# Optimization experiments

Measured on AMD Instinct MI355X. Metric: run time of the kernel, lower is better.

The kernel has to match this reference:

```python
import jax, jax.numpy as jnp
import numpy as np

K = 20          # neighbors
BN_EPS = 1e-5


def _knn_idx(x, k):
    """x: [B, C, N] -> idx of k nearest neighbors [B, N, k] (by squared distance, self included)."""
    xx = jnp.sum(x * x, axis=1)                       # [B, N]
    inner = jnp.einsum('bcn,bcm->bnm', x, x)          # [B, N, N]
    neg_sqdist = 2.0 * inner - xx[:, :, None] - xx[:, None, :]
    return jax.lax.top_k(neg_sqdist, k)[1]            # [B, N, k]


def _graph_feature(x, k):
    """x: [B, C, N] -> edge features cat(x_j - x_i, x_i): [B, 2C, N, k]."""
    idx = _knn_idx(x, k)                              # [B, N, k]
    xT = x.transpose(0, 2, 1)                         # [B, N, C]
    nbrs = jax.vmap(lambda xt, ii: xt[ii])(xT, idx)   # [B, N, k, C] gather
    center = xT[:, :, None, :]                        # [B, N, 1, C]
    feat = jnp.concatenate(
        [nbrs - center, jnp.broadcast_to(center, nbrs.shape)], axis=-1)  # [B, N, k, 2C]
    return feat.transpose(0, 3, 1, 2)                 # [B, 2C, N, k]


def _conv_bn_lrelu(feat, W, gamma, beta, mean, var):
    """1x1 Conv2d (no bias) + BatchNorm (given stats) + LeakyReLU(0.2). feat: [B, Cin, N, k]."""
    y = jnp.einsum('oc,bcnk->bonk', W, feat)
    scale = (gamma / jnp.sqrt(var + BN_EPS))[None, :, None, None]
    y = (y - mean[None, :, None, None]) * scale + beta[None, :, None, None]
    return jnp.where(y > 0, y, 0.2 * y)


def setup_inputs() -> dict:
    key = jax.random.key(0)
    ks = list(jax.random.split(key, 32))
    B, N = 8, 1024
    f32 = jnp.float32

    def w(kk, o, i):
        return jax.random.normal(kk, (o, i), dtype=f32) / np.sqrt(i)

    def bn(k1, k2, k3, k4, c):
        g = jax.random.uniform(k1, (c,), dtype=f32, minval=0.5, maxval=1.5)
        b = jax.random.normal(k2, (c,), dtype=f32) * 0.05
        m = jax.random.normal(k3, (c,), dtype=f32) * 0.05
        v = jax.random.uniform(k4, (c,), dtype=f32, minval=0.5, maxval=1.5)
        return g, b, m, v

    x = jax.random.normal(ks[0], (B, N, 3), dtype=f32)
    W0 = w(ks[1], 64, 6);    g0, b0, m0, v0 = bn(ks[2], ks[3], ks[4], ks[5], 64)
    W1 = w(ks[6], 128, 128); g1, b1, m1, v1 = bn(ks[7], ks[8], ks[9], ks[10], 128)
    W2 = w(ks[11], 256, 256); g2, b2, m2, v2 = bn(ks[12], ks[13], ks[14], ks[15], 256)
    Wf = w(ks[16], 512, 896); gf, bf, mf, vf = bn(ks[17], ks[18], ks[19], ks[20], 512)
    We = w(ks[21], 256, 512)
    return dict(x=x,
                W0=W0, g0=g0, b0=b0, m0=m0, v0=v0,
                W1=W1, g1=g1, b1=b1, m1=m1, v1=v1,
                W2=W2, g2=g2, b2=b2, m2=m2, v2=v2,
                Wf=Wf, gf=gf, bf=bf, mf=mf, vf=vf,
                We=We)


def reference(x, W0, g0, b0, m0, v0, W1, g1, b1, m1, v1,
              W2, g2, b2, m2, v2, Wf, gf, bf, mf, vf, We):
    h = x.transpose(0, 2, 1)                          # [B, 3, N]
    outs = []
    for (W, g, b, m, v) in ((W0, g0, b0, m0, v0),
                            (W1, g1, b1, m1, v1),
                            (W2, g2, b2, m2, v2)):
        gfeat = _graph_feature(h, K)                  # [B, 2C, N, k]
        y = _conv_bn_lrelu(gfeat, W, g, b, m, v)      # [B, Cout, N, k]
        h = y.mean(axis=-1)                           # max-free EdgeConv pool over k
        outs.append(h)
    cat = jnp.concatenate(outs, axis=1)               # [B, 448, N]
    gfeat = _graph_feature(cat, K)                    # [B, 896, N, k]
    y = _conv_bn_lrelu(gfeat, Wf, gf, bf, mf, vf)     # [B, 512, N, k]
    pooled = y.mean(axis=-1).mean(axis=-1)            # [B, 512] (pool over k then N)
    return pooled @ We.T                              # [B, num_features]
```

## Files before the change

### kernel.cpp

```cpp
#include <hip/hip_runtime.h>
#include <cstdint>

#define KNN 20
#define BV 8
#define NV 1024

template <int CTRL>
__device__ __forceinline__ unsigned dppmax(unsigned x) {
    unsigned m = (unsigned)__builtin_amdgcn_update_dpp((int)x, (int)x, CTRL, 0xf, 0xf, false);
    return (x > m) ? x : m;
}
template <int CTRL>
__device__ __forceinline__ unsigned dppmin(unsigned x) {
    unsigned m = (unsigned)__builtin_amdgcn_update_dpp((int)x, (int)x, CTRL, 0xf, 0xf, false);
    return (x < m) ? x : m;
}
__device__ __forceinline__ unsigned wave_max_u32(unsigned x) {
    x = dppmax<0xB1>(x); x = dppmax<0x4E>(x); x = dppmax<0x141>(x);
    x = dppmax<0x140>(x); x = dppmax<0x142>(x); x = dppmax<0x143>(x);
    return (unsigned)__builtin_amdgcn_readlane((int)x, 63);
}
__device__ __forceinline__ unsigned wave_min_u32(unsigned x) {
    x = dppmin<0xB1>(x); x = dppmin<0x4E>(x); x = dppmin<0x141>(x);
    x = dppmin<0x140>(x); x = dppmin<0x142>(x); x = dppmin<0x143>(x);
    return (unsigned)__builtin_amdgcn_readlane((int)x, 63);
}

__global__ __launch_bounds__(256) void k_transpose(const float* __restrict__ x, float* __restrict__ hx) {
    int id = blockIdx.x * 256 + threadIdx.x;
    if (id >= BV * 3 * NV) return;
    int n = id % NV;
    int c = (id / NV) % 3;
    int b = id / (3 * NV);
    hx[id] = x[(b * NV + n) * 3 + c];
}

__global__ __launch_bounds__(256) void k_xx(const float* __restrict__ h, float* __restrict__ xx,
                                            int C, int bstride) {
    int id = blockIdx.x * 256 + threadIdx.x;
    int n = id % NV, b = id / NV;
    if (b >= BV) return;
    const float* hp = h + (size_t)b * bstride + n;
    float s = 0.f;
    for (int c = 0; c < C; ++c) { float v = hp[(size_t)c * NV]; s += v * v; }
    xx[b * NV + n] = s;
}

__global__ __launch_bounds__(512, 4) void k_knn(const float* __restrict__ h, const float* __restrict__ xx,
                                                int C, int bstride, int* __restrict__ idx) {
    __shared__ float Bs[8][1024];
    const int bx = blockIdx.x;
    const int b = bx & 7, tile = bx >> 3;
    const int i0 = tile * 16;
    const int t = threadIdx.x, lane = t & 63, w = t >> 6;
    const int irow = i0 + w * 2;
    float acc[2][16] = {};
    const float* hb = h + (size_t)b * bstride;

    for (int c0 = 0; c0 < C; c0 += 8) {
        __syncthreads();
#pragma unroll
        for (int r = 0; r < 4; ++r) {
            int e = r * 512 + t;
            int cc = e >> 8, jj = e & 255;
            float4 v = make_float4(0.f, 0.f, 0.f, 0.f);
            if (c0 + cc < C) v = *(const float4*)&hb[(size_t)(c0 + cc) * NV + jj * 4];
            *(float4*)&Bs[cc][jj * 4] = v;
        }
        __syncthreads();
#pragma unroll
        for (int c = 0; c < 8; ++c) {
            float2 arv = *(const float2*)&Bs[c][irow];
            float ar[2] = {arv.x, arv.y};
            float br[16];
#pragma unroll
            for (int g = 0; g < 4; ++g) {
                float4 bv = *(const float4*)&Bs[c][g * 256 + (lane << 2)];
                br[g * 4 + 0] = bv.x; br[g * 4 + 1] = bv.y;
                br[g * 4 + 2] = bv.z; br[g * 4 + 3] = bv.w;
            }
#pragma unroll
            for (int a = 0; a < 2; ++a)
#pragma unroll
                for (int q = 0; q < 16; ++q) acc[a][q] += ar[a] * br[q];
        }
    }

    const float* xb = xx + b * NV;
    float xxj[16];
#pragma unroll
    for (int g = 0; g < 4; ++g) {
        float4 xv = *(const float4*)&xb[g * 256 + (lane << 2)];
        xxj[g * 4 + 0] = xv.x; xxj[g * 4 + 1] = xv.y;
        xxj[g * 4 + 2] = xv.z; xxj[g * 4 + 3] = xv.w;
    }
    unsigned ua[2][16];
#pragma unroll
    for (int a = 0; a < 2; ++a) {
        float xi = xb[irow + a];
#pragma unroll
        for (int q = 0; q < 16; ++q) {
            float d = 2.f * acc[a][q] - xi - xxj[q];
            unsigned u = __float_as_uint(d);
            ua[a][q] = ((int)u < 0) ? ~u : (u | 0x80000000u);
        }
    }

    int* opb = idx + ((size_t)(b * NV + irow)) * KNN;
#pragma unroll 1
    for (int s = 0; s < KNN; ++s) {
#pragma unroll
        for (int a = 0; a < 2; ++a) {
            unsigned w0[8]; int p0[8];
#pragma unroll
            for (int i = 0; i < 8; ++i) {
                bool g = ua[a][2 * i + 1] > ua[a][2 * i];
                w0[i] = g ? ua[a][2 * i + 1] : ua[a][2 * i];
                p0[i] = g ? 2 * i + 1 : 2 * i;
            }
            unsigned w1[4]; int p1[4];
#pragma unroll
            for (int i = 0; i < 4; ++i) {
                bool g = w1[0], gg = w0[2 * i + 1] > w0[2 * i];
                (void)g;
                w1[i] = gg ? w0[2 * i + 1] : w0[2 * i];
                p1[i] = gg ? p0[2 * i + 1] : p0[2 * i];
            }
            unsigned w2[2]; int p2[2];
#pragma unroll
            for (int i = 0; i < 2; ++i) {
                bool gg = w1[2 * i + 1] > w1[2 * i];
                w2[i] = gg ? w1[2 * i + 1] : w1[2 * i];
                p2[i] = gg ? p1[2 * i + 1] : p1[2 * i];
            }
            bool gf = w2[1] > w2[0];
            unsigned su = gf ? w2[1] : w2[0];
            int bq = gf ? p2[1] : p2[0];

            unsigned gmax = wave_max_u32(su);
            int myj = ((bq >> 2) << 8) + (lane << 2) + (bq & 3);
            unsigned cand = (su == gmax) ? (unsigned)myj : 0xFFFFFFFFu;
            int j = (int)wave_min_u32(cand);
            if (lane == 0) opb[a * KNN + s] = j;
            int wq = (cand == (unsigned)j) ? bq : 99;
#pragma unroll
            for (int q = 0; q < 16; ++q)
                if (wq == q) ua[a][q] = 0u;
        }
    }
}

__global__ __launch_bounds__(256) void k_pack(const float* __restrict__ W, float* __restrict__ wb,
                                              int C, int O) {
    int id = blockIdx.x * 256 + threadIdx.x;
    if (id >= 2 * O * C) return;
    int c = id % C, o = (id / C) % O, half = id / (C * O);
    float wl = W[(size_t)o * 2 * C + c];
    wb[id] = half ? (W[(size_t)o * 2 * C + C + c] - wl) : wl;
}

__global__ __launch_bounds__(256) void k_gemm(const float* __restrict__ A, int astride,
                                              const float* __restrict__ h, int bstride, int C,
                                              float* __restrict__ out, int O) {
    __shared__ float Ws[8][64], Hs[8][128];
    const int b = blockIdx.x, n0 = blockIdx.y * 128, o0 = blockIdx.z * 64;
    const int t = threadIdx.x, tx = t & 15, ty = t >> 4;
    float acc[4][8] = {};
    const float* hb = h + (size_t)b * bstride;
    for (int c0 = 0; c0 < C; c0 += 8) {
#pragma unroll
        for (int q = 0; q < 2; ++q) {
            int e = t + q * 256;
            int oo = e >> 3, cc = e & 7;
            Ws[cc][oo] = ((c0 + cc) < C) ? A[(size_t)(o0 + oo) * astride + c0 + cc] : 0.f;
        }
        {
            int cc = t >> 5, nn4 = t & 31;
            float4 v = make_float4(0.f, 0.f, 0.f, 0.f);
            if (c0 + cc < C) v = *(const float4*)&hb[(size_t)(c0 + cc) * NV + n0 + nn4 * 4];
            *(float4*)&Hs[cc][nn4 * 4] = v;
        }
        __syncthreads();
#pragma unroll
        for (int c = 0; c < 8; ++c) {
            float4 wv = *(const float4*)&Ws[c][ty * 4];
            float ar[4] = {wv.x, wv.y, wv.z, wv.w};
            float br[8];
            float4 h0 = *(const float4*)&Hs[c][tx * 4];
            float4 h1 = *(const float4*)&Hs[c][64 + tx * 4];
            br[0] = h0.x; br[1] = h0.y; br[2] = h0.z; br[3] = h0.w;
            br[4] = h1.x; br[5] = h1.y; br[6] = h1.z; br[7] = h1.w;
#pragma unroll
            for (int a = 0; a < 4; ++a)
#pragma unroll
                for (int q = 0; q < 8; ++q) acc[a][q] += ar[a] * br[q];
        }
        __syncthreads();
    }
#pragma unroll
    for (int a = 0; a < 4; ++a) {
        int o = o0 + ty * 4 + a;
        float* outp = out + ((size_t)b * O + o) * NV + n0;
        float4 s0 = make_float4(acc[a][0], acc[a][1], acc[a][2], acc[a][3]);
        float4 s1 = make_float4(acc[a][4], acc[a][5], acc[a][6], acc[a][7]);
        *(float4*)&outp[tx * 4] = s0;
        *(float4*)&outp[64 + tx * 4] = s1;
    }
}

__global__ __launch_bounds__(256) void k_edge(const float* __restrict__ pd,
                                              const int* __restrict__ idx,
                                              const float* __restrict__ ga, const float* __restrict__ be,
                                              const float* __restrict__ mu, const float* __restrict__ va,
                                              float* __restrict__ out, int out_bstride, int O) {
    const int b = blockIdx.x;
    const int n = blockIdx.y * 256 + threadIdx.x;
    const int o0 = blockIdx.z * 4;
    const int* ip = idx + ((size_t)b * NV + n) * KNN;
    int jj[KNN];
#pragma unroll
    for (int k = 0; k < KNN; ++k) jj[k] = ip[k];
#pragma unroll
    for (int a = 0; a < 4; ++a) {
        const int o = o0 + a;
        const float al = ga[o] / sqrtf(va[o] + 1e-5f);
        const float c0 = be[o] - mu[o] * al;
        const float* pb = pd + ((size_t)b * 2 * O + o) * NV;
        const float dv  = pd[((size_t)b * 2 * O + O + o) * NV + n];
        float s = 0.f;
#pragma unroll
        for (int k = 0; k < KNN; ++k) {
            float y = fmaf(al, pb[jj[k]] + dv, c0);
            s += (y > 0.f) ? y : 0.2f * y;
        }
        out[(size_t)b * out_bstride + (size_t)o * NV + n] = s * (1.f / KNN);
    }
}

__global__ __launch_bounds__(256) void k_pool(const float* __restrict__ hf, float* __restrict__ pooled) {
    const int o = blockIdx.x, b = blockIdx.y;
    const float* hp = hf + ((size_t)b * 512 + o) * NV;
    float s = 0.f;
    for (int i = threadIdx.x; i < NV; i += 256) s += hp[i];
#pragma unroll
    for (int off = 32; off > 0; off >>= 1) s += __shfl_down(s, off, 64);
    __shared__ float red[4];
    if ((threadIdx.x & 63) == 0) red[threadIdx.x >> 6] = s;
    __syncthreads();
    if (threadIdx.x == 0)
        pooled[(size_t)b * 512 + o] = (red[0] + red[1] + red[2] + red[3]) * (1.f / NV);
}

__global__ __launch_bounds__(256) void k_final(const float* __restrict__ pooled, const float* __restrict__ We,
                                               float* __restrict__ out) {
    const int j = threadIdx.x, b = blockIdx.x;
    __shared__ float ps[512];
    for (int o = threadIdx.x; o < 512; o += 256) ps[o] = pooled[b * 512 + o];
    __syncthreads();
    float s = 0.f;
    for (int o = 0; o < 512; ++o) s += ps[o] * We[(size_t)j * 512 + o];
    out[b * 256 + j] = s;
}

extern "C" void kernel_launch(void* const* d_in, const int* in_sizes, int n_in,
                              void* d_out, int out_size, void* d_ws, size_t ws_size,
                              hipStream_t stream) {
    const float* x  = (const float*)d_in[0];
    const float* W0 = (const float*)d_in[1];
    const float* g0 = (const float*)d_in[2];
    const float* b0 = (const float*)d_in[3];
    const float* m0 = (const float*)d_in[4];
    const float* v0 = (const float*)d_in[5];
    const float* W1 = (const float*)d_in[6];
    const float* g1 = (const float*)d_in[7];
    const float* b1 = (const float*)d_in[8];
    const float* m1 = (const float*)d_in[9];
    const float* v1 = (const float*)d_in[10];
    const float* W2 = (const float*)d_in[11];
    const float* g2 = (const float*)d_in[12];
    const float* b2 = (const float*)d_in[13];
    const float* m2 = (const float*)d_in[14];
    const float* v2 = (const float*)d_in[15];
    const float* Wf = (const float*)d_in[16];
    const float* gf = (const float*)d_in[17];
    const float* bf = (const float*)d_in[18];
    const float* mf = (const float*)d_in[19];
    const float* vf = (const float*)d_in[20];
    const float* We = (const float*)d_in[21];

    float* ws = (float*)d_ws;
    float* hx     = ws;
    float* cat    = hx + 24576;
    float* xx     = cat + 3670016;
    int*   idx    = (int*)(xx + 8192);
    float* pd     = (float*)(idx + 163840);
    float* wb     = pd + 8388608;
    float* hf     = wb + 458752;
    float* pooled = hf + 4194304;

    k_transpose<<<96, 256, 0, stream>>>(x, hx);

    auto run_layer = [&](const float* h, int C, int bstride, const float* W,
                         const float* g, const float* be, const float* m, const float* v,
                         int O, float* outp, int obstride) {
        k_xx<<<32, 256, 0, stream>>>(h, xx, C, bstride);
        k_knn<<<512, 512, 0, stream>>>(h, xx, C, bstride, idx);
        int pn = 2 * O * C;
        k_pack<<<(pn + 255) / 256, 256, 0, stream>>>(W, wb, C, O);
        k_gemm<<<dim3(8, 8, 2 * O / 64), 256, 0, stream>>>(wb, C, h, bstride, C, pd, 2 * O);
        k_edge<<<dim3(8, 4, O / 4), 256, 0, stream>>>(pd, idx, g, be, m, v, outp, obstride, O);
    };

    run_layer(hx, 3, 3 * NV, W0, g0, b0, m0, v0, 64, cat, 448 * NV);
    run_layer(cat, 64, 448 * NV, W1, g1, b1, m1, v1, 128, cat + 64 * NV, 448 * NV);
    run_layer(cat + 64 * NV, 128, 448 * NV, W2, g2, b2, m2, v2, 256, cat + 192 * NV, 448 * NV);
    run_layer(cat, 448, 448 * NV, Wf, gf, bf, mf, vf, 512, hf, 512 * NV);

    k_pool<<<dim3(512, 8), 256, 0, stream>>>(hf, pooled);
    k_final<<<8, 256, 0, stream>>>(pooled, We, (float*)d_out);
}
```

Before: 802.6 us.

## Split kNN columns across wave halves and merge per-half top-k in shared memory

The kNN kernel now gives each wave 4 query rows over half of the candidate columns, instead of 2 rows over all 1024. Each wave selects a top-20 per row within its half. The two sorted half-lists are then merged through shared memory by 16 threads. The selection compares floats directly instead of order-preserving unsigned keys, and the occupancy hint in the launch bounds is lowered. Per-lane reduction work shrinks, but the number of wave-wide DPP reductions per block doubles and a serial merge step is added.

```diff
diff --git a/kernel.cpp b/kernel.cpp
--- a/kernel.cpp
+++ b/kernel.cpp
@@ -6,19 +6,20 @@
 #define NV 1024
 
 template <int CTRL>
-__device__ __forceinline__ unsigned dppmax(unsigned x) {
-    unsigned m = (unsigned)__builtin_amdgcn_update_dpp((int)x, (int)x, CTRL, 0xf, 0xf, false);
-    return (x > m) ? x : m;
+__device__ __forceinline__ float dppmaxf(float x) {
+    int xi = __float_as_int(x);
+    int mi = __builtin_amdgcn_update_dpp(xi, xi, CTRL, 0xf, 0xf, false);
+    return fmaxf(x, __int_as_float(mi));
 }
 template <int CTRL>
 __device__ __forceinline__ unsigned dppmin(unsigned x) {
     unsigned m = (unsigned)__builtin_amdgcn_update_dpp((int)x, (int)x, CTRL, 0xf, 0xf, false);
     return (x < m) ? x : m;
 }
-__device__ __forceinline__ unsigned wave_max_u32(unsigned x) {
-    x = dppmax<0xB1>(x); x = dppmax<0x4E>(x); x = dppmax<0x141>(x);
-    x = dppmax<0x140>(x); x = dppmax<0x142>(x); x = dppmax<0x143>(x);
-    return (unsigned)__builtin_amdgcn_readlane((int)x, 63);
+__device__ __forceinline__ float wave_max_f32(float x) {
+    x = dppmaxf<0xB1>(x); x = dppmaxf<0x4E>(x); x = dppmaxf<0x141>(x);
+    x = dppmaxf<0x140>(x); x = dppmaxf<0x142>(x); x = dppmaxf<0x143>(x);
+    return __int_as_float(__builtin_amdgcn_readlane(__float_as_int(x), 63));
 }
 __device__ __forceinline__ unsigned wave_min_u32(unsigned x) {
     x = dppmin<0xB1>(x); x = dppmin<0x4E>(x); x = dppmin<0x141>(x);
@@ -46,15 +47,19 @@
     xx[b * NV + n] = s;
 }
 
-__global__ __launch_bounds__(512, 4) void k_knn(const float* __restrict__ h, const float* __restrict__ xx,
+__global__ __launch_bounds__(512, 2) void k_knn(const float* __restrict__ h, const float* __restrict__ xx,
                                                 int C, int bstride, int* __restrict__ idx) {
     __shared__ float Bs[8][1024];
+    __shared__ float sv[16][2][KNN];
+    __shared__ int   sj[16][2][KNN];
     const int bx = blockIdx.x;
     const int b = bx & 7, tile = bx >> 3;
     const int i0 = tile * 16;
     const int t = threadIdx.x, lane = t & 63, w = t >> 6;
-    const int irow = i0 + w * 2;
-    float acc[2][16] = {};
+    const int rg = w & 3, hf = w >> 2;
+    const int irow = i0 + rg * 4;
+    const int jb = hf * 512;
+    float acc[4][8] = {};
     const float* hb = h + (size_t)b * bstride;
 
     for (int c0 = 0; c0 < C; c0 += 8) {
@@ -70,82 +75,90 @@
         __syncthreads();
 #pragma unroll
         for (int c = 0; c < 8; ++c) {
-            float2 arv = *(const float2*)&Bs[c][irow];
-            float ar[2] = {arv.x, arv.y};
-            float br[16];
-#pragma unroll
-            for (int g = 0; g < 4; ++g) {
-                float4 bv = *(const float4*)&Bs[c][g * 256 + (lane << 2)];
+            float4 arv = *(const float4*)&Bs[c][irow];
+            float ar[4] = {arv.x, arv.y, arv.z, arv.w};
+            float br[8];
+#pragma unroll
+            for (int g = 0; g < 2; ++g) {
+                float4 bv = *(const float4*)&Bs[c][jb + g * 256 + (lane << 2)];
                 br[g * 4 + 0] = bv.x; br[g * 4 + 1] = bv.y;
                 br[g * 4 + 2] = bv.z; br[g * 4 + 3] = bv.w;
             }
 #pragma unroll
-            for (int a = 0; a < 2; ++a)
-#pragma unroll
-                for (int q = 0; q < 16; ++q) acc[a][q] += ar[a] * br[q];
+            for (int a = 0; a < 4; ++a)
+#pragma unroll
+                for (int q = 0; q < 8; ++q) acc[a][q] += ar[a] * br[q];
         }
     }
 
     const float* xb = xx + b * NV;
-    float xxj[16];
-#pragma unroll
-    for (int g = 0; g < 4; ++g) {
-        float4 xv = *(const float4*)&xb[g * 256 + (lane << 2)];
+    float xxj[8];
+#pragma unroll
+    for (int g = 0; g < 2; ++g) {
+        float4 xv = *(const float4*)&xb[jb + g * 256 + (lane << 2)];
         xxj[g * 4 + 0] = xv.x; xxj[g * 4 + 1] = xv.y;
         xxj[g * 4 + 2] = xv.z; xxj[g * 4 + 3] = xv.w;
     }
-    unsigned ua[2][16];
-#pragma unroll
-    for (int a = 0; a < 2; ++a) {
+#pragma unroll
+    for (int a = 0; a < 4; ++a) {
         float xi = xb[irow + a];
 #pragma unroll
-        for (int q = 0; q < 16; ++q) {
-            float d = 2.f * acc[a][q] - xi - xxj[q];
-            unsigned u = __float_as_uint(d);
-            ua[a][q] = ((int)u < 0) ? ~u : (u | 0x80000000u);
-        }
-    }
-
-    int* opb = idx + ((size_t)(b * NV + irow)) * KNN;
+        for (int q = 0; q < 8; ++q) acc[a][q] = 2.f * acc[a][q] - xi - xxj[q];
+    }
+
 #pragma unroll 1
     for (int s = 0; s < KNN; ++s) {
 #pragma unroll
-        for (int a = 0; a < 2; ++a) {
-            unsigned w0[8]; int p0[8];
-#pragma unroll
-            for (int i = 0; i < 8; ++i) {
-                bool g = ua[a][2 * i + 1] > ua[a][2 * i];
-                w0[i] = g ? ua[a][2 * i + 1] : ua[a][2 * i];
+        for (int a = 0; a < 4; ++a) {
+            float w0[4]; int p0[4];
+#pragma unroll
+            for (int i = 0; i < 4; ++i) {
+                bool g = acc[a][2 * i + 1] > acc[a][2 * i];
+                w0[i] = g ? acc[a][2 * i + 1] : acc[a][2 * i];
                 p0[i] = g ? 2 * i + 1 : 2 * i;
             }
-            unsigned w1[4]; int p1[4];
-#pragma unroll
-            for (int i = 0; i < 4; ++i) {
-                bool g = w1[0], gg = w0[2 * i + 1] > w0[2 * i];
-                (void)g;
-                w1[i] = gg ? w0[2 * i + 1] : w0[2 * i];
-                p1[i] = gg ? p0[2 * i + 1] : p0[2 * i];
+            float w1[2]; int p1[2];
+#pragma unroll
+            for (int i = 0; i < 2; ++i) {
+                bool g = w0[2 * i + 1] > w0[2 * i];
+                w1[i] = g ? w0[2 * i + 1] : w0[2 * i];
+                p1[i] = g ? p0[2 * i + 1] : p0[2 * i];
             }
-            unsigned w2[2]; int p2[2];
-#pragma unroll
-            for (int i = 0; i < 2; ++i) {
-                bool gg = w1[2 * i + 1] > w1[2 * i];
-                w2[i] = gg ? w1[2 * i + 1] : w1[2 * i];
-                p2[i] = gg ? p1[2 * i + 1] : p1[2 * i];
+            bool gf = w1[1] > w1[0];
+            float bv = gf ? w1[1] : w1[0];
+            int bq = gf ? p1[1] : p1[0];
+
+            float gmax = wave_max_f32(bv);
+            int myj = jb + ((bq >> 2) << 8) + (lane << 2) + (bq & 3);
+            unsigned cand = (bv == gmax) ? (unsigned)myj : 0xFFFFFFFFu;
+            int j = (int)wave_min_u32(cand);
+            if (lane == 0) {
+                sv[rg * 4 + a][hf][s] = gmax;
+                sj[rg * 4 + a][hf][s] = j;
             }
-            bool gf = w2[1] > w2[0];
-            unsigned su = gf ? w2[1] : w2[0];
-            int bq = gf ? p2[1] : p2[0];
-
-            unsigned gmax = wave_max_u32(su);
-            int myj = ((bq >> 2) << 8) + (lane << 2) + (bq & 3);
-            unsigned cand = (su == gmax) ? (unsigned)myj : 0xFFFFFFFFu;
-            int j = (int)wave_min_u32(cand);
-            if (lane == 0) opb[a * KNN + s] = j;
             int wq = (cand == (unsigned)j) ? bq : 99;
 #pragma unroll
-            for (int q = 0; q < 16; ++q)
-                if (wq == q) ua[a][q] = 0u;
+            for (int q = 0; q < 8; ++q)
+                if (wq == q) acc[a][q] = -3.4e38f;
+        }
+    }
+
+    __syncthreads();
+    if (t < 16) {
+        const float* v0 = sv[t][0];
+        const float* v1 = sv[t][1];
+        const int* j0 = sj[t][0];
+        const int* j1 = sj[t][1];
+        int* op = idx + ((size_t)(b * NV + i0 + t)) * KNN;
+        int a = 0, c2 = 0;
+#pragma unroll
+        for (int s = 0; s < KNN; ++s) {
+            float va = v0[a], vb = v1[c2];
+            int ja = j0[a], jb2 = j1[c2];
+            bool take0 = (va > vb) || (va == vb && ja < jb2);
+            op[s] = take0 ? ja : jb2;
+            a += take0 ? 1 : 0;
+            c2 += take0 ? 0 : 1;
         }
     }
 }
```

Result: slower. 846.0 us (+5.4%).
